# Kernel optimization log

Hardware: AMD Instinct MI355X
Metric: run time of the kernel (lower is better)

## Reference

```python
import jax, jax.numpy as jnp
import numpy as np

N_NODES = 50000
N_EDGES = 800000
IN_FEATS = 256
N_HEADS = 4
OUT_FEATS = 32
NEG_SLOPE = 0.2


def setup_inputs() -> dict:
    key = jax.random.key(0)
    k_feat, k_src, k_dst, k_fc, k_al, k_ar, k_res = jax.random.split(key, 7)
    feat = jax.random.normal(k_feat, (N_NODES, IN_FEATS), dtype=jnp.float32)
    src = jax.random.randint(k_src, (N_EDGES,), 0, N_NODES)
    dst = jax.random.randint(k_dst, (N_EDGES,), 0, N_NODES)
    # xavier-normal-ish scales
    s_fc = (2.0 / (IN_FEATS + N_HEADS * OUT_FEATS)) ** 0.5
    W_fc = jax.random.normal(k_fc, (N_HEADS * OUT_FEATS, IN_FEATS), dtype=jnp.float32) * s_fc
    s_a = (2.0 / (1 + N_HEADS * OUT_FEATS)) ** 0.5
    attn_l = jax.random.normal(k_al, (N_HEADS, OUT_FEATS), dtype=jnp.float32) * s_a
    attn_r = jax.random.normal(k_ar, (N_HEADS, OUT_FEATS), dtype=jnp.float32) * s_a
    W_res = jax.random.normal(k_res, (N_HEADS * OUT_FEATS, IN_FEATS), dtype=jnp.float32) * s_fc
    return {"feat": feat, "src": src, "dst": dst, "W_fc": W_fc,
            "attn_l": attn_l, "attn_r": attn_r, "W_res": W_res}


def reference(feat, src, dst, W_fc, attn_l, attn_r, W_res):
    N = feat.shape[0]
    H, D = attn_l.shape
    ones_e = jnp.ones(src.shape[0], dtype=feat.dtype)

    # projection: [N, H, D]
    h = (feat @ W_fc.T).reshape(N, H, D)
    feat_dst = h  # dst features are pre-norm (torch code aliases before * norm)

    # symmetric norm on source side: out_degree^-0.5
    out_deg = jax.ops.segment_sum(ones_e, src, num_segments=N)
    feat_src = h * (jnp.clip(out_deg, 1.0) ** -0.5)[:, None, None]

    # per-node attention halves -> per-edge score, leaky relu
    el = jnp.einsum('nhd,hd->nh', feat_src, attn_l)  # [N, H]
    er = jnp.einsum('nhd,hd->nh', feat_dst, attn_r)  # [N, H]
    e = jax.nn.leaky_relu(el[src] + er[dst], NEG_SLOPE)  # [E, H]

    # edge_softmax over incoming edges of each dst node
    emax = jax.ops.segment_max(e, dst, num_segments=N)
    emax = jnp.where(jnp.isfinite(emax), emax, 0.0)  # guard empty segments
    ex = jnp.exp(e - emax[dst])
    denom = jax.ops.segment_sum(ex, dst, num_segments=N)
    a = ex / denom[dst]  # [E, H]

    # weighted scatter-sum of messages: u_mul_e + sum
    msg = feat_src[src] * a[:, :, None]  # [E, H, D]
    rst = jax.ops.segment_sum(msg, dst, num_segments=N)  # [N, H, D]

    # symmetric norm on destination side: in_degree^0.5
    in_deg = jax.ops.segment_sum(ones_e, dst, num_segments=N)
    rst = rst * jnp.sqrt(jnp.clip(in_deg, 1.0))[:, None, None]

    # residual projection
    rst = rst + (feat @ W_res.T).reshape(N, H, D)
    return rst
```

## Files before the change

### kernel.cpp

```cpp
#include <hip/hip_runtime.h>
#include <hip/hip_bf16.h>
#include <math.h>

#define HD 128
#define IN_F 256
#define NEG_SLOPE 0.2f
#define NMAX 50000
#define GGRID 256
#define CSRC 32

typedef __attribute__((ext_vector_type(8))) short short8;
typedef __attribute__((ext_vector_type(4))) float f32x4;

__device__ __forceinline__ unsigned short f2bf(float x) {
    __hip_bfloat16 b = __float2bfloat16(x);
    return *(unsigned short*)&b;
}
__device__ __forceinline__ float bf2f(unsigned short u) {
    unsigned int v = ((unsigned int)u) << 16;
    float f;
    __builtin_memcpy(&f, &v, 4);
    return f;
}
__device__ __forceinline__ short8 pack8(float4 f0, float4 f1) {
    short8 v;
    v[0] = (short)f2bf(f0.x); v[1] = (short)f2bf(f0.y);
    v[2] = (short)f2bf(f0.z); v[3] = (short)f2bf(f0.w);
    v[4] = (short)f2bf(f1.x); v[5] = (short)f2bf(f1.y);
    v[6] = (short)f2bf(f1.z); v[7] = (short)f2bf(f1.w);
    return v;
}

__global__ __launch_bounds__(256) void cvt_ew_kernel(
    const float4* __restrict__ wfc4, const float4* __restrict__ wres4,
    const float* __restrict__ wfc, const float* __restrict__ attn_l,
    const float* __restrict__ attn_r, ushort4* __restrict__ w16,
    unsigned short* __restrict__ ew16, int n4each) {
    int b = blockIdx.x;
    if (b < 4) {
        int h = b, k = threadIdx.x;
        float sl = 0.f, sr = 0.f;
#pragma unroll 8
        for (int d = 0; d < 32; d++) {
            float w = wfc[(size_t)(h * 32 + d) * IN_F + k];
            sl += attn_l[h * 32 + d] * w;
            sr += attn_r[h * 32 + d] * w;
        }
        ew16[h * IN_F + k] = f2bf(sl);
        ew16[(4 + h) * IN_F + k] = f2bf(sr);
        ew16[(8 + h) * IN_F + k] = 0;
        ew16[(12 + h) * IN_F + k] = 0;
        return;
    }
    int idx = (b - 4) * 256 + threadIdx.x;
    if (idx >= 2 * n4each) return;
    float4 f = (idx < n4each) ? wfc4[idx] : wres4[idx - n4each];
    ushort4 u;
    u.x = f2bf(f.x); u.y = f2bf(f.y); u.z = f2bf(f.z); u.w = f2bf(f.w);
    w16[idx] = u;
}

__global__ __launch_bounds__(1024) void hist_kernel(const int* __restrict__ src,
                                                    const int* __restrict__ dst,
                                                    unsigned short* __restrict__ pc_src,
                                                    unsigned short* __restrict__ pc_dst,
                                                    int N, int E, int C, int chunk,
                                                    int chunk_s) {
    __shared__ unsigned int h[NMAX / 2];
    int tid = threadIdx.x;
    int nh = N >> 1;
    uint4* h4 = (uint4*)h;
    for (int i = tid; i < (nh >> 2); i += 1024) h4[i] = make_uint4(0, 0, 0, 0);
    for (int i = (nh & ~3) + tid; i < nh; i += 1024) h[i] = 0;
    __syncthreads();

    int b = blockIdx.x;
    bool isSrc = (b >= C);
    const int* arr = isSrc ? src : dst;
    int c = isSrc ? (b - C) : b;
    int ch = isSrc ? chunk_s : chunk;
    int e0 = c * ch, e1 = min(E, (c + 1) * ch);
    for (int e = e0 + tid; e < e1; e += 1024) {
        int v = arr[e];
        atomicAdd(&h[v >> 1], 1u << ((v & 1) << 4));
    }
    __syncthreads();

    unsigned short* pc = (isSrc ? pc_src : pc_dst) + (size_t)c * N;
    uint4* pc4 = (uint4*)pc;
    for (int i = tid; i < (nh >> 2); i += 1024) pc4[i] = h4[i];
    for (int i = (nh & ~3) + tid; i < nh; i += 1024) ((unsigned int*)pc)[i] = h[i];
}

__global__ __launch_bounds__(256) void sum_scan1_kernel(
    const unsigned short* __restrict__ pc_src, unsigned short* __restrict__ pc_dst,
    int* __restrict__ out_cnt, int* __restrict__ deg, int* __restrict__ bsum,
    int N, int C) {
    __shared__ int wsum[4];
    int n = blockIdx.x * 256 + threadIdx.x;
    int sd = 0;
    if (n < N) {
        int ss = 0;
#pragma unroll 4
        for (int c = 0; c < CSRC; c++) ss += pc_src[(size_t)c * N + n];
        for (int c = 0; c < C; c++) {
            unsigned short v = pc_dst[(size_t)c * N + n];
            pc_dst[(size_t)c * N + n] = (unsigned short)sd;
            sd += v;
        }
        out_cnt[n] = ss;
        deg[n] = sd;
    }
    int v = (n < N) ? sd : 0;
#pragma unroll
    for (int d = 1; d < 64; d <<= 1) v += __shfl_xor(v, d);
    if ((threadIdx.x & 63) == 0) wsum[threadIdx.x >> 6] = v;
    __syncthreads();
    if (threadIdx.x == 0) bsum[blockIdx.x] = wsum[0] + wsum[1] + wsum[2] + wsum[3];
}

__global__ __launch_bounds__(256) void scan3_kernel(const int* __restrict__ deg,
                                                    const int* __restrict__ bsum,
                                                    int* __restrict__ row_start,
                                                    int N, int nb, int E) {
    __shared__ int wsum[4];
    __shared__ int sbo[256];
    int tid = threadIdx.x, lane = tid & 63, wid = tid >> 6;
    {
        int v = (tid < nb) ? bsum[tid] : 0;
        int incl = v;
#pragma unroll
        for (int d = 1; d < 64; d <<= 1) {
            int t = __shfl_up(incl, d);
            if (lane >= d) incl += t;
        }
        if (lane == 63) wsum[wid] = incl;
        __syncthreads();
        int woff = 0;
        for (int w = 0; w < wid; w++) woff += wsum[w];
        sbo[tid] = woff + incl - v;
        __syncthreads();
    }
    int boff = sbo[blockIdx.x];
    if (blockIdx.x == 0 && tid == 0) row_start[N] = E;
    __syncthreads();

    int i = blockIdx.x * 256 + tid;
    int v = (i < N) ? deg[i] : 0;
    int incl = v;
#pragma unroll
    for (int d = 1; d < 64; d <<= 1) {
        int t = __shfl_up(incl, d);
        if (lane >= d) incl += t;
    }
    if (lane == 63) wsum[wid] = incl;
    __syncthreads();
    int woff = 0;
    for (int w = 0; w < wid; w++) woff += wsum[w];
    int excl = boff + woff + incl - v;
    if (i < N) row_start[i] = excl;
}

__global__ __launch_bounds__(1024) void place_kernel(const int* __restrict__ src,
                                                     const int* __restrict__ dst,
                                                     const unsigned short* __restrict__ chunkpre,
                                                     const int* __restrict__ row_start,
                                                     int* __restrict__ esrc,
                                                     int N, int E, int chunk) {
    __shared__ unsigned int cur[NMAX / 2];
    int tid = threadIdx.x;
    int nh = N >> 1;
    const unsigned short* cp = chunkpre + (size_t)blockIdx.x * N;
    const uint4* cp4 = (const uint4*)cp;
    uint4* cur4 = (uint4*)cur;
    for (int i = tid; i < (nh >> 2); i += 1024) cur4[i] = cp4[i];
    for (int i = (nh & ~3) + tid; i < nh; i += 1024) cur[i] = ((const unsigned int*)cp)[i];
    __syncthreads();

    int e1 = min(E, (int)(blockIdx.x + 1) * chunk);
    for (int e = blockIdx.x * chunk + tid; e < e1; e += 1024) {
        int d = dst[e], s = src[e];
        int sh = (d & 1) << 4;
        unsigned int old = atomicAdd(&cur[d >> 1], 1u << sh);
        int rank = (old >> sh) & 0xffff;
        esrc[row_start[d] + rank] = s;
    }
}

__global__ __launch_bounds__(1024, 1) void gemm_fused(
    const float* __restrict__ feat, const __hip_bfloat16* __restrict__ w16,
    const __hip_bfloat16* __restrict__ ew16, const int* __restrict__ out_cnt,
    unsigned short* __restrict__ h16, unsigned short* __restrict__ resid16,
    float* __restrict__ el, float* __restrict__ er, int N, int ntiles) {
    __shared__ unsigned short sB[256 * 256];
    __shared__ unsigned short sA[32 * 256];
    int tid = threadIdx.x;
    int lane = tid & 63, w = tid >> 6;
    int l15 = lane & 15, lg = lane >> 4;
    int c0 = w * 16;
    bool w0 = (w == 0);
    bool isH = (w < 8);
    int colloc = c0 & 127;

#pragma unroll
    for (int it = 0; it < 8; ++it) {
        int idx = it * 1024 + tid;
        int c = idx >> 5, g = idx & 31;
        short8 v = *(const short8*)(w16 + (size_t)c * IN_F + g * 8);
        *(short8*)&sB[c * 256 + ((g ^ (c & 7)) * 8)] = v;
    }
    short8 ereg[8];
    if (w0) {
        const __hip_bfloat16* ep = ew16 + (size_t)l15 * IN_F + lg * 8;
#pragma unroll
        for (int kk = 0; kk < 8; kk++) ereg[kk] = *(const short8*)(ep + kk * 32);
    }

    int srow = tid >> 5, sgc = tid & 31;

    float4 fA0, fA1;
    int t = blockIdx.x;
    {
        int gm = t * 32 + srow;
        gm = (gm < N) ? gm : (N - 1);
        const float4* fp = (const float4*)(feat + (size_t)gm * IN_F + sgc * 8);
        fA0 = fp[0];
        fA1 = fp[1];
    }

    for (; t < ntiles; t += GGRID) {
        __syncthreads();
        *(short8*)&sA[srow * 256 + ((sgc ^ (srow & 7)) * 8)] = pack8(fA0, fA1);
        __syncthreads();

        int tn = t + GGRID;
        if (tn < ntiles) {
            int gm = tn * 32 + srow;
            gm = (gm < N) ? gm : (N - 1);
            const float4* fp = (const float4*)(feat + (size_t)gm * IN_F + sgc * 8);
            fA0 = fp[0];
            fA1 = fp[1];
        }

        f32x4 acc[2], accE[2];
#pragma unroll
        for (int i = 0; i < 2; i++) {
            acc[i] = (f32x4){0.f, 0.f, 0.f, 0.f};
            accE[i] = (f32x4){0.f, 0.f, 0.f, 0.f};
        }
#pragma unroll
        for (int kk = 0; kk < 8; kk++) {
            short8 a[2], b;
#pragma unroll
            for (int mi = 0; mi < 2; mi++) {
                int row = mi * 16 + l15;
                int gs = (kk * 4 + lg) ^ (row & 7);
                a[mi] = *(const short8*)&sA[row * 256 + gs * 8];
            }
            {
                int c = c0 + l15;
                int gsb = (kk * 4 + lg) ^ (c & 7);
                b = *(const short8*)&sB[c * 256 + gsb * 8];
            }
#pragma unroll
            for (int mi = 0; mi < 2; mi++)
                acc[mi] = __builtin_amdgcn_mfma_f32_16x16x32_bf16(a[mi], b, acc[mi],
                                                                  0, 0, 0);
            if (w0) {
#pragma unroll
                for (int mi = 0; mi < 2; mi++)
                    accE[mi] = __builtin_amdgcn_mfma_f32_16x16x32_bf16(
                        a[mi], ereg[kk], accE[mi], 0, 0, 0);
            }
        }

        int bm = t * 32;
#pragma unroll
        for (int mi = 0; mi < 2; mi++) {
#pragma unroll
            for (int reg = 0; reg < 4; reg++) {
                int r = bm + mi * 16 + lg * 4 + reg;
                bool valid = (r < N);
                int rr = valid ? r : 0;
                if (isH) {
                    float nrm = rsqrtf(fmaxf((float)out_cnt[rr], 1.0f));
                    if (valid) {
                        h16[(size_t)r * HD + colloc + l15] =
                            f2bf(acc[mi][reg] * nrm);
                        if (w0) {
                            float ev = accE[mi][reg];
                            if (l15 < 4) el[r * 4 + l15] = ev * nrm;
                            else if (l15 < 8) er[r * 4 + (l15 - 4)] = ev;
                        }
                    }
                } else if (valid) {
                    resid16[(size_t)r * HD + colloc + l15] = f2bf(acc[mi][reg]);
                }
            }
        }
    }
}

__global__ __launch_bounds__(256) void agg_kernel(const unsigned short* __restrict__ h16,
                                                  const float* __restrict__ el,
                                                  const float* __restrict__ er,
                                                  const int* __restrict__ row_start,
                                                  const int* __restrict__ esrc,
                                                  const unsigned short* __restrict__ resid16,
                                                  float* __restrict__ out, int N) {
    int wid = threadIdx.x >> 6, lane = threadIdx.x & 63;
    int n = blockIdx.x * 4 + wid;
    if (n >= N) return;
    int es = lane >> 4;
    int l15 = lane & 15;
    int h = l15 >> 2;
    int d0 = l15 * 8;
    int beg = row_start[n], end = row_start[n + 1];
    float erh = er[n * 4 + h];
    float den = 0.f;
    float acc[8];
#pragma unroll
    for (int j = 0; j < 8; j++) acc[j] = 0.f;

    if (beg < end) {
        bool ok0, ok1;
        float ev0, ev1; short8 hv0, hv1;
        {
            int i0 = beg + es, i1 = beg + 4 + es;
            ok0 = i0 < end; ok1 = i1 < end;
            int s0 = esrc[ok0 ? i0 : beg];
            int s1 = esrc[ok1 ? i1 : beg];
            ev0 = el[s0 * 4 + h]; ev1 = el[s1 * 4 + h];
            hv0 = *(const short8*)(h16 + (size_t)s0 * HD + d0);
            hv1 = *(const short8*)(h16 + (size_t)s1 * HD + d0);
        }
        for (int base = beg + 8; base < end; base += 8) {
            int i0 = base + es, i1 = base + 4 + es;
            bool p0 = i0 < end, p1 = i1 < end;
            int t0 = esrc[p0 ? i0 : beg];
            int t1 = esrc[p1 ? i1 : beg];
            float fv0 = el[t0 * 4 + h];
            float fv1 = el[t1 * 4 + h];
            short8 g0 = *(const short8*)(h16 + (size_t)t0 * HD + d0);
            short8 g1 = *(const short8*)(h16 + (size_t)t1 * HD + d0);
            float e0 = ev0 + erh; e0 = (e0 > 0.f) ? e0 : NEG_SLOPE * e0;
            float e1 = ev1 + erh; e1 = (e1 > 0.f) ? e1 : NEG_SLOPE * e1;
            float ex0 = ok0 ? __expf(e0) : 0.f;
            float ex1 = ok1 ? __expf(e1) : 0.f;
            den += ex0 + ex1;
#pragma unroll
            for (int j = 0; j < 8; j++)
                acc[j] += ex0 * bf2f((unsigned short)hv0[j]) +
                          ex1 * bf2f((unsigned short)hv1[j]);
            ok0 = p0; ok1 = p1; ev0 = fv0; ev1 = fv1; hv0 = g0; hv1 = g1;
        }
        float e0 = ev0 + erh; e0 = (e0 > 0.f) ? e0 : NEG_SLOPE * e0;
        float e1 = ev1 + erh; e1 = (e1 > 0.f) ? e1 : NEG_SLOPE * e1;
        float ex0 = ok0 ? __expf(e0) : 0.f;
        float ex1 = ok1 ? __expf(e1) : 0.f;
        den += ex0 + ex1;
#pragma unroll
        for (int j = 0; j < 8; j++)
            acc[j] += ex0 * bf2f((unsigned short)hv0[j]) +
                      ex1 * bf2f((unsigned short)hv1[j]);
    }

#pragma unroll
    for (int m = 16; m < 64; m <<= 1) {
        den += __shfl_xor(den, m);
#pragma unroll
        for (int j = 0; j < 8; j++) acc[j] += __shfl_xor(acc[j], m);
    }

    if (es == 0) {
        const unsigned short* rp = resid16 + (size_t)n * HD + d0;
        short8 rv = *(const short8*)rp;
        int indeg = end - beg;
        float sc = (indeg > 0) ? sqrtf((float)indeg) / den : 0.f;
        float o[8];
#pragma unroll
        for (int j = 0; j < 8; j++)
            o[j] = sc * acc[j] + bf2f((unsigned short)rv[j]);
        float* op = out + (size_t)n * HD + d0;
        *(float4*)op = make_float4(o[0], o[1], o[2], o[3]);
        *(float4*)(op + 4) = make_float4(o[4], o[5], o[6], o[7]);
    }
}

extern "C" void kernel_launch(void* const* d_in, const int* in_sizes, int n_in,
                              void* d_out, int out_size, void* d_ws, size_t ws_size,
                              hipStream_t stream) {
    const float* feat   = (const float*)d_in[0];
    const int*   src    = (const int*)d_in[1];
    const int*   dst    = (const int*)d_in[2];
    const float* W_fc   = (const float*)d_in[3];
    const float* attn_l = (const float*)d_in[4];
    const float* attn_r = (const float*)d_in[5];
    const float* W_res  = (const float*)d_in[6];
    float* out = (float*)d_out;

    int N = in_sizes[0] / IN_F;
    int E = in_sizes[1];
    int nb = (N + 255) / 256;

    size_t off = 0;
    auto alloc = [&](size_t bytes) {
        size_t o = off;
        off = (off + bytes + 255) & ~(size_t)255;
        return o;
    };
    char* ws = (char*)d_ws;
    unsigned short* h16     = (unsigned short*)(ws + alloc((size_t)N * HD * 2));
    unsigned short* resid16 = (unsigned short*)(ws + alloc((size_t)N * HD * 2));
    __hip_bfloat16* w16     = (__hip_bfloat16*)(ws + alloc((size_t)2 * HD * IN_F * 2));
    unsigned short* ew16    = (unsigned short*)(ws + alloc((size_t)16 * IN_F * 2));
    float* el               = (float*)(ws + alloc((size_t)N * 4 * 4));
    float* er               = (float*)(ws + alloc((size_t)N * 4 * 4));
    int* out_cnt            = (int*)(ws + alloc((size_t)N * 4));
    int* deg                = (int*)(ws + alloc((size_t)N * 4));
    int* row_start          = (int*)(ws + alloc((size_t)(N + 1) * 4));
    int* bsum               = (int*)(ws + alloc((size_t)nb * 4));
    int* esrc               = (int*)(ws + alloc((size_t)E * 4));
    unsigned short* pc_src  = (unsigned short*)(ws + alloc((size_t)CSRC * N * 2));

    size_t per_chunk = (size_t)2 * N;
    size_t avail = (ws_size > off + 4096) ? (ws_size - off - 4096) : 0;
    int C = (int)(avail / per_chunk);
    if (C > 128) C = 128;
    if (C < 32) C = 32;
    unsigned short* pc_dst = (unsigned short*)(ws + alloc((size_t)C * N * 2));
    int chunk = (E + C - 1) / C;
    int chunk_s = (E + CSRC - 1) / CSRC;

    int n4each = HD * IN_F / 4;
    int cvtb = (2 * n4each + 255) / 256;
    cvt_ew_kernel<<<4 + cvtb, 256, 0, stream>>>(
        (const float4*)W_fc, (const float4*)W_res, W_fc, attn_l, attn_r,
        (ushort4*)w16, ew16, n4each);

    hist_kernel<<<C + CSRC, 1024, 0, stream>>>(src, dst, pc_src, pc_dst,
                                               N, E, C, chunk, chunk_s);
    sum_scan1_kernel<<<nb, 256, 0, stream>>>(pc_src, pc_dst, out_cnt, deg, bsum, N, C);
    scan3_kernel<<<nb, 256, 0, stream>>>(deg, bsum, row_start, N, nb, E);
    place_kernel<<<C, 1024, 0, stream>>>(src, dst, pc_dst, row_start, esrc, N, E, chunk);

    int ntiles = (N + 31) / 32;
    gemm_fused<<<GGRID, 1024, 0, stream>>>(feat, (const __hip_bfloat16*)w16,
                                           (const __hip_bfloat16*)ew16, out_cnt,
                                           h16, resid16, el, er, N, ntiles);

    int nb4 = (N + 3) / 4;
    agg_kernel<<<nb4, 256, 0, stream>>>(h16, el, er, row_start, esrc, resid16, out, N);
}
```

Before: 141.5 us.

## Merge weight conversion into histogram kernel and CSR placement into GEMM kernel

Folds the weight bf16 conversion and attention-vector projection into the histogram launch as extra blocks, and runs the CSR edge placement as extra blocks of the fused projection GEMM launch. This removes two kernel launches and lets independent work overlap on the GPU instead of serializing. The merged kernel uses a shared 144KB LDS union, so place blocks now reserve more LDS than before, and GEMM blocks may start behind place blocks, which can change how well the two kinds of work share the compute units.

```diff
diff --git a/kernel.cpp b/kernel.cpp
--- a/kernel.cpp
+++ b/kernel.cpp
@@ -31,50 +31,51 @@
     return v;
 }
 
-__global__ __launch_bounds__(256) void cvt_ew_kernel(
+__global__ __launch_bounds__(1024) void hist_cvt_kernel(
+    const int* __restrict__ src, const int* __restrict__ dst,
+    unsigned short* __restrict__ pc_src, unsigned short* __restrict__ pc_dst,
     const float4* __restrict__ wfc4, const float4* __restrict__ wres4,
     const float* __restrict__ wfc, const float* __restrict__ attn_l,
     const float* __restrict__ attn_r, ushort4* __restrict__ w16,
-    unsigned short* __restrict__ ew16, int n4each) {
-    int b = blockIdx.x;
-    if (b < 4) {
-        int h = b, k = threadIdx.x;
-        float sl = 0.f, sr = 0.f;
-#pragma unroll 8
-        for (int d = 0; d < 32; d++) {
-            float w = wfc[(size_t)(h * 32 + d) * IN_F + k];
-            sl += attn_l[h * 32 + d] * w;
-            sr += attn_r[h * 32 + d] * w;
-        }
-        ew16[h * IN_F + k] = f2bf(sl);
-        ew16[(4 + h) * IN_F + k] = f2bf(sr);
-        ew16[(8 + h) * IN_F + k] = 0;
-        ew16[(12 + h) * IN_F + k] = 0;
-        return;
-    }
-    int idx = (b - 4) * 256 + threadIdx.x;
-    if (idx >= 2 * n4each) return;
-    float4 f = (idx < n4each) ? wfc4[idx] : wres4[idx - n4each];
-    ushort4 u;
-    u.x = f2bf(f.x); u.y = f2bf(f.y); u.z = f2bf(f.z); u.w = f2bf(f.w);
-    w16[idx] = u;
-}
-
-__global__ __launch_bounds__(1024) void hist_kernel(const int* __restrict__ src,
-                                                    const int* __restrict__ dst,
-                                                    unsigned short* __restrict__ pc_src,
-                                                    unsigned short* __restrict__ pc_dst,
-                                                    int N, int E, int C, int chunk,
-                                                    int chunk_s) {
+    unsigned short* __restrict__ ew16, int n4each,
+    int N, int E, int C, int chunk, int chunk_s) {
     __shared__ unsigned int h[NMAX / 2];
     int tid = threadIdx.x;
+    int b = blockIdx.x;
+
+    if (b >= C + CSRC) {
+        int rb = b - C - CSRC;
+        if (rb == 0) {
+            int hh = tid >> 8, k = tid & 255;
+            float sl = 0.f, sr = 0.f;
+#pragma unroll 8
+            for (int d = 0; d < 32; d++) {
+                float w = wfc[(size_t)(hh * 32 + d) * IN_F + k];
+                sl += attn_l[hh * 32 + d] * w;
+                sr += attn_r[hh * 32 + d] * w;
+            }
+            ew16[hh * IN_F + k] = f2bf(sl);
+            ew16[(4 + hh) * IN_F + k] = f2bf(sr);
+            ew16[(8 + hh) * IN_F + k] = 0;
+            ew16[(12 + hh) * IN_F + k] = 0;
+        } else {
+            int idx = (rb - 1) * 1024 + tid;
+            if (idx < 2 * n4each) {
+                float4 f = (idx < n4each) ? wfc4[idx] : wres4[idx - n4each];
+                ushort4 u;
+                u.x = f2bf(f.x); u.y = f2bf(f.y); u.z = f2bf(f.z); u.w = f2bf(f.w);
+                w16[idx] = u;
+            }
+        }
+        return;
+    }
+
     int nh = N >> 1;
     uint4* h4 = (uint4*)h;
     for (int i = tid; i < (nh >> 2); i += 1024) h4[i] = make_uint4(0, 0, 0, 0);
     for (int i = (nh & ~3) + tid; i < nh; i += 1024) h[i] = 0;
     __syncthreads();
 
-    int b = blockIdx.x;
     bool isSrc = (b >= C);
     const int* arr = isSrc ? src : dst;
     int c = isSrc ? (b - C) : b;
@@ -161,40 +162,43 @@
     if (i < N) row_start[i] = excl;
 }
 
-__global__ __launch_bounds__(1024) void place_kernel(const int* __restrict__ src,
-                                                     const int* __restrict__ dst,
-                                                     const unsigned short* __restrict__ chunkpre,
-                                                     const int* __restrict__ row_start,
-                                                     int* __restrict__ esrc,
-                                                     int N, int E, int chunk) {
-    __shared__ unsigned int cur[NMAX / 2];
-    int tid = threadIdx.x;
-    int nh = N >> 1;
-    const unsigned short* cp = chunkpre + (size_t)blockIdx.x * N;
-    const uint4* cp4 = (const uint4*)cp;
-    uint4* cur4 = (uint4*)cur;
-    for (int i = tid; i < (nh >> 2); i += 1024) cur4[i] = cp4[i];
-    for (int i = (nh & ~3) + tid; i < nh; i += 1024) cur[i] = ((const unsigned int*)cp)[i];
-    __syncthreads();
-
-    int e1 = min(E, (int)(blockIdx.x + 1) * chunk);
-    for (int e = blockIdx.x * chunk + tid; e < e1; e += 1024) {
-        int d = dst[e], s = src[e];
-        int sh = (d & 1) << 4;
-        unsigned int old = atomicAdd(&cur[d >> 1], 1u << sh);
-        int rank = (old >> sh) & 0xffff;
-        esrc[row_start[d] + rank] = s;
-    }
-}
-
-__global__ __launch_bounds__(1024, 1) void gemm_fused(
+__global__ __launch_bounds__(1024, 1) void place_gemm_kernel(
+    const int* __restrict__ src, const int* __restrict__ dst,
+    const unsigned short* __restrict__ chunkpre, const int* __restrict__ row_start,
+    int* __restrict__ esrc,
     const float* __restrict__ feat, const __hip_bfloat16* __restrict__ w16,
     const __hip_bfloat16* __restrict__ ew16, const int* __restrict__ out_cnt,
     unsigned short* __restrict__ h16, unsigned short* __restrict__ resid16,
-    float* __restrict__ el, float* __restrict__ er, int N, int ntiles) {
-    __shared__ unsigned short sB[256 * 256];
-    __shared__ unsigned short sA[32 * 256];
+    float* __restrict__ el, float* __restrict__ er,
+    int N, int E, int C, int chunk, int ntiles) {
+    __shared__ __align__(16) char smem[147456];
     int tid = threadIdx.x;
+
+    if (blockIdx.x < C) {
+        unsigned int* cur = (unsigned int*)smem;
+        int nh = N >> 1;
+        const unsigned short* cp = chunkpre + (size_t)blockIdx.x * N;
+        const uint4* cp4 = (const uint4*)cp;
+        uint4* cur4 = (uint4*)cur;
+        for (int i = tid; i < (nh >> 2); i += 1024) cur4[i] = cp4[i];
+        for (int i = (nh & ~3) + tid; i < nh; i += 1024)
+            cur[i] = ((const unsigned int*)cp)[i];
+        __syncthreads();
+
+        int e1 = min(E, (int)(blockIdx.x + 1) * chunk);
+        for (int e = blockIdx.x * chunk + tid; e < e1; e += 1024) {
+            int d = dst[e], s = src[e];
+            int sh = (d & 1) << 4;
+            unsigned int old = atomicAdd(&cur[d >> 1], 1u << sh);
+            int rank = (old >> sh) & 0xffff;
+            esrc[row_start[d] + rank] = s;
+        }
+        return;
+    }
+
+    unsigned short* sB = (unsigned short*)smem;
+    unsigned short* sA = (unsigned short*)(smem + 131072);
+    int bid = blockIdx.x - C;
     int lane = tid & 63, w = tid >> 6;
     int l15 = lane & 15, lg = lane >> 4;
     int c0 = w * 16;
@@ -217,9 +221,8 @@
     }
 
     int srow = tid >> 5, sgc = tid & 31;
-
     float4 fA0, fA1;
-    int t = blockIdx.x;
+    int t = bid;
     {
         int gm = t * 32 + srow;
         gm = (gm < N) ? gm : (N - 1);
@@ -285,8 +288,7 @@
                 if (isH) {
                     float nrm = rsqrtf(fmaxf((float)out_cnt[rr], 1.0f));
                     if (valid) {
-                        h16[(size_t)r * HD + colloc + l15] =
-                            f2bf(acc[mi][reg] * nrm);
+                        h16[(size_t)r * HD + colloc + l15] = f2bf(acc[mi][reg] * nrm);
                         if (w0) {
                             float ev = accE[mi][reg];
                             if (l15 < 4) el[r * 4 + l15] = ev * nrm;
@@ -433,21 +435,21 @@
     int chunk_s = (E + CSRC - 1) / CSRC;
 
     int n4each = HD * IN_F / 4;
-    int cvtb = (2 * n4each + 255) / 256;
-    cvt_ew_kernel<<<4 + cvtb, 256, 0, stream>>>(
+    int cvtb = (2 * n4each + 1023) / 1024;
+
+    hist_cvt_kernel<<<C + CSRC + 1 + cvtb, 1024, 0, stream>>>(
+        src, dst, pc_src, pc_dst,
         (const float4*)W_fc, (const float4*)W_res, W_fc, attn_l, attn_r,
-        (ushort4*)w16, ew16, n4each);
-
-    hist_kernel<<<C + CSRC, 1024, 0, stream>>>(src, dst, pc_src, pc_dst,
-                                               N, E, C, chunk, chunk_s);
+        (ushort4*)w16, ew16, n4each, N, E, C, chunk, chunk_s);
+
     sum_scan1_kernel<<<nb, 256, 0, stream>>>(pc_src, pc_dst, out_cnt, deg, bsum, N, C);
     scan3_kernel<<<nb, 256, 0, stream>>>(deg, bsum, row_start, N, nb, E);
-    place_kernel<<<C, 1024, 0, stream>>>(src, dst, pc_dst, row_start, esrc, N, E, chunk);
 
     int ntiles = (N + 31) / 32;
-    gemm_fused<<<GGRID, 1024, 0, stream>>>(feat, (const __hip_bfloat16*)w16,
-                                           (const __hip_bfloat16*)ew16, out_cnt,
-                                           h16, resid16, el, er, N, ntiles);
+    place_gemm_kernel<<<C + GGRID, 1024, 0, stream>>>(
+        src, dst, pc_dst, row_start, esrc,
+        feat, (const __hip_bfloat16*)w16, (const __hip_bfloat16*)ew16, out_cnt,
+        h16, resid16, el, er, N, E, C, chunk, ntiles);
 
     int nb4 = (N + 3) / 4;
     agg_kernel<<<nb4, 256, 0, stream>>>(h16, el, er, row_start, esrc, resid16, out, N);
```

After: 133.2 us. -5.9%, faster.
